# Optimization experiments

Measured on AMD Instinct MI355X. Metric: run time of the kernel, lower is better.

## Reference

```python
import jax, jax.numpy as jnp
import numpy as np

N_FFT = 1024
HOP_LENGTH = 480
NB_MAX_FRAMES = 1000
N_MELS = 64
SPEC_WIDTH = 1024
N_BINS = N_FFT // 2 + 1  # 513


def setup_inputs() -> dict:
    key = jax.random.key(0)
    B, L = 32, 480000  # 10 s @ 48 kHz -> 1001 frames, truncated to 1000
    waveform = jax.random.normal(key, (B, L), dtype=jnp.float32)

    # DFT-as-conv weights, exactly as in the torch module (hann periodic window)
    n = np.arange(N_FFT, dtype=np.float32)
    window = 0.5 - 0.5 * np.cos(2.0 * np.pi * n / N_FFT)  # torch.hann_window (periodic)
    k = np.arange(N_BINS, dtype=np.float32)[:, None]
    angle = 2.0 * np.pi * k * n[None, :] / N_FFT
    stft_weights = np.concatenate(
        [window * np.cos(angle), -window * np.sin(angle)], axis=0
    ).astype(np.float32)  # [2*N_BINS, N_FFT]

    # Stand-in for HF's slaney mel filterbank (513 -> 64): non-negative, sparse-ish scale
    mel_filters = jax.random.uniform(
        jax.random.fold_in(key, 1), (N_BINS, N_MELS), dtype=jnp.float32
    ) * 0.02

    return {
        "waveform": waveform,
        "stft_weights": jnp.asarray(stft_weights),
        "mel_filters": mel_filters,
    }


def _bilinear_align_corners(img, out_h, out_w):
    """F.interpolate(mode='bilinear', align_corners=True) on [B,C,H,W]."""
    B, C, H, W = img.shape

    def coords(out, inn):
        scale = (inn - 1) / max(out - 1, 1)
        pos = jnp.arange(out, dtype=jnp.float32) * scale
        i0 = jnp.clip(jnp.floor(pos).astype(jnp.int32), 0, inn - 1)
        return i0, pos - i0.astype(jnp.float32)

    h0, hw = coords(out_h, H)
    w0, ww = coords(out_w, W)
    h1 = jnp.minimum(h0 + 1, H - 1)
    w1 = jnp.minimum(w0 + 1, W - 1)

    rows = (img[:, :, h0, :] * (1.0 - hw)[None, None, :, None]
            + img[:, :, h1, :] * hw[None, None, :, None])  # [B,C,out_h,W]
    out = rows[..., w0] * (1.0 - ww) + rows[..., w1] * ww   # [B,C,out_h,out_w]
    return out


def reference(waveform, stft_weights, mel_filters):
    pad = N_FFT // 2
    x = jnp.pad(waveform, ((0, 0), (pad, pad)), mode="reflect")  # center=True

    # strided conv1d == frame extraction + GEMM with the DFT matrix
    T = (x.shape[1] - N_FFT) // HOP_LENGTH + 1
    idx = jnp.arange(T)[:, None] * HOP_LENGTH + jnp.arange(N_FFT)[None, :]
    frames = x[:, idx]                                   # [B, T, N_FFT]
    spec = jnp.einsum("btn,kn->bkt", frames, stft_weights)  # [B, 2*N_BINS, T]

    real = spec[:, :N_BINS, :]
    imag = spec[:, N_BINS:, :]
    power = (real * real + imag * imag)[:, :, :NB_MAX_FRAMES]  # [B, 513, 1000]

    mel = jnp.einsum("bft,fm->bmt", power, mel_filters)        # [B, 64, 1000]
    log_mel = 10.0 * jnp.log10(jnp.clip(mel, 1e-10))

    img = jnp.transpose(log_mel, (0, 2, 1))[:, None]           # [B, 1, 1000, 64]
    return _bilinear_align_corners(img, SPEC_WIDTH, N_MELS)    # [B, 1, 1024, 64]
```

## Files before the change

### kernel.cpp

```cpp
#include <hip/hip_runtime.h>
#include <hip/hip_bf16.h>
#include <math.h>

#define LWAV   480000
#define XHALF  240512
#define NBATCH 32
#define TOUT   1000
#define NMEL   64
#define PSTR   576
#define SPECW  1024

#define XPE_OFF  0u
#define XPO_OFF  15392768u
#define WEO_OFF  30785536u
#define WMT_OFF  31834112u
#define PW_OFF   31907840u
#define LM_OFF   68771840u
#define W256_OFF 76963840u

typedef __attribute__((ext_vector_type(8))) __bf16 bf16x8;
typedef __attribute__((ext_vector_type(8))) unsigned short ushort8;
typedef __attribute__((ext_vector_type(4))) float  f32x4;

__device__ __forceinline__ void gload16(const void* g, void* l) {
  __builtin_amdgcn_global_load_lds((const __attribute__((address_space(1))) void*)g,
                                   (__attribute__((address_space(3))) void*)l, 16, 0, 0);
}
#define WAIT_VM(n)  asm volatile("s_waitcnt vmcnt(" #n ")" ::: "memory")
#define WAIT_LGKM0  asm volatile("s_waitcnt lgkmcnt(0)" ::: "memory")
#define BAR() __builtin_amdgcn_s_barrier()

__device__ __forceinline__ float bf2f(unsigned short u) {
  return __uint_as_float((unsigned)u << 16);
}

#define NG1 (NBATCH * (XHALF / 8))
#define NG2 ((1024 * 512) / 8)
#define NG3 ((NMEL * PSTR) / 8)
#define NG4 (1024 / 8)

__global__ void prep_kernel(const float* __restrict__ wav,
                            const float* __restrict__ wstft,
                            const float* __restrict__ mf,
                            unsigned char* __restrict__ ws) {
  __hip_bfloat16* xpE = (__hip_bfloat16*)(ws + XPE_OFF);
  __hip_bfloat16* xpO = (__hip_bfloat16*)(ws + XPO_OFF);
  __hip_bfloat16* weo = (__hip_bfloat16*)(ws + WEO_OFF);
  __hip_bfloat16* wmt = (__hip_bfloat16*)(ws + WMT_OFF);
  __hip_bfloat16* w256 = (__hip_bfloat16*)(ws + W256_OFF);
  int idx = blockIdx.x * blockDim.x + threadIdx.x;
  if (idx < NG1) {
    int b = idx / (XHALF / 8);
    int g = idx - b * (XHALF / 8);
    const float* src = wav + (size_t)b * LWAV;
    __hip_bfloat16 e[8], o[8];
    if (g >= 32 && g <= 30030) {
      const float4* p = (const float4*)(src + 16 * g - 512);
#pragma unroll
      for (int u = 0; u < 4; ++u) {
        float4 v = p[u];
        e[2 * u]     = __float2bfloat16(v.x);
        o[2 * u]     = __float2bfloat16(v.y);
        e[2 * u + 1] = __float2bfloat16(v.z);
        o[2 * u + 1] = __float2bfloat16(v.w);
      }
    } else {
      for (int i = 0; i < 16; ++i) {
        int q = 16 * g + i;
        int s = q - 512;
        if (s < 0) s = -s;
        else if (s >= LWAV) s = 2 * (LWAV - 1) - s;
        __hip_bfloat16 v = __float2bfloat16(src[s]);
        if (i & 1) o[i >> 1] = v; else e[i >> 1] = v;
      }
    }
    *(uint4*)(xpE + (size_t)b * XHALF + 8 * g) = *(const uint4*)e;
    *(uint4*)(xpO + (size_t)b * XHALF + 8 * g) = *(const uint4*)o;
  } else if (idx < NG1 + NG2) {
    int v = idx - NG1;
    int row = v >> 6;
    int mseg = (v & 63) * 8;
    int comp = row >> 8, j = row & 255;
    __hip_bfloat16 t[8];
    if (comp < 2) {
      const float4* srow = (const float4*)(wstft + (size_t)(comp == 0 ? j : 513 + j) * 1024 + 2 * mseg);
#pragma unroll
      for (int u = 0; u < 4; ++u) {
        float4 vv = srow[u];
        t[2 * u]     = __float2bfloat16(vv.x);
        t[2 * u + 1] = __float2bfloat16(vv.z);
      }
    } else {
      const float4* w0 = (const float4*)(wstft + 2 * mseg);
#pragma unroll
      for (int u = 0; u < 4; ++u) {
        float4 wwv = w0[u];
        float wo[2] = {wwv.y, wwv.w};
#pragma unroll
        for (int h = 0; h < 2; ++h) {
          int mm = mseg + 2 * u + h;
          int q = (j * mm) & 511;
          float ang = (float)q * 0.012271846f;
          float val = (comp == 2) ? wo[h] * cosf(ang) : -wo[h] * sinf(ang);
          t[2 * u + h] = __float2bfloat16(val);
        }
      }
    }
    *(uint4*)(weo + (size_t)row * 512 + mseg) = *(const uint4*)t;
  } else if (idx < NG1 + NG2 + NG3) {
    int j = idx - NG1 - NG2;
    int n = j / (PSTR / 8);
    int k0 = (j - n * (PSTR / 8)) * 8;
    for (int k = k0; k < k0 + 8; ++k)
      wmt[n * PSTR + k] = __float2bfloat16(k < 513 ? mf[k * NMEL + n] : 0.0f);
  } else if (idx < NG1 + NG2 + NG3 + NG4) {
    int j = idx - NG1 - NG2 - NG3;
    int part = j >> 6;
    int m0 = (j & 63) * 8;
    __hip_bfloat16 t[8];
#pragma unroll
    for (int h = 0; h < 8; ++h) {
      int m = m0 + h;
      float v = part == 0 ? wstft[(size_t)256 * 1024 + 2 * m]
                          : wstft[(size_t)769 * 1024 + 2 * m + 1];
      t[h] = __float2bfloat16(v);
    }
    *(uint4*)(w256 + part * 512 + m0) = *(const uint4*)t;
  }
}

__launch_bounds__(256, 2)
__global__ void p256_kernel(unsigned char* __restrict__ ws) {
  __hip_bfloat16* pw = (__hip_bfloat16*)(ws + PW_OFF);
  const int tid  = threadIdx.x;
  const int l16  = tid & 15;
  const int fidx = blockIdx.x * 16 + (tid >> 4);
  const int b = fidx / 1000, t = fidx - b * 1000;

  const unsigned short* xe = (const unsigned short*)(ws + XPE_OFF) +
      (size_t)b * XHALF + 240 * (size_t)t + l16 * 32;
  const unsigned short* xo = (const unsigned short*)(ws + XPO_OFF) +
      (size_t)b * XHALF + 240 * (size_t)t + l16 * 32;
  const unsigned short* we = (const unsigned short*)(ws + W256_OFF) + l16 * 32;
  const unsigned short* wo = (const unsigned short*)(ws + W256_OFF) + 512 + l16 * 32;

  ushort8 ev[4], ov[4], wev[4], wov[4];
#pragma unroll
  for (int q = 0; q < 4; ++q) {
    ev[q]  = *(const ushort8*)(xe + q * 8);
    ov[q]  = *(const ushort8*)(xo + q * 8);
    wev[q] = *(const ushort8*)(we + q * 8);
    wov[q] = *(const ushort8*)(wo + q * 8);
  }
  float dc = 0.f, ds = 0.f;
#pragma unroll
  for (int q = 0; q < 4; ++q)
#pragma unroll
    for (int u = 0; u < 8; ++u) {
      dc += bf2f(ev[q][u]) * bf2f(wev[q][u]);
      ds += bf2f(ov[q][u]) * bf2f(wov[q][u]);
    }
#pragma unroll
  for (int d = 1; d < 16; d <<= 1) {
    dc += __shfl_xor(dc, d);
    ds += __shfl_xor(ds, d);
  }
  if (l16 == 0)
    pw[((size_t)b * TOUT + t) * PSTR + 256] = __float2bfloat16(dc * dc + ds * ds);
}

#define STFT_NWG 1000
__launch_bounds__(256, 2)
__global__ void stft_kernel(unsigned char* __restrict__ ws) {
  __shared__ __align__(16) unsigned char lds[65536];
  __hip_bfloat16* pw = (__hip_bfloat16*)(ws + PW_OFF);

  const int tid  = threadIdx.x;
  const int lane = tid & 63;
  const int w    = tid >> 6;
  const int wm   = w >> 1;
  const int wn   = w & 1;

  const int orig = blockIdx.x;
  const int wg = (orig & 7) * 125 + (orig >> 3);
  const int j0 = (wg & 3) * 64;
  const int m0 = (wg >> 2) * 128;

  const unsigned char* gsA[4];
  {
    int sl  = tid & 7;
    int rq  = tid >> 3;
    int slp = sl ^ (rq & 7);
#pragma unroll
    for (int i = 0; i < 4; ++i) {
      int row = i * 32 + rq;
      int m = m0 + row;
      int bb = m / 1000, tt = m - bb * 1000;
      size_t fb = ((size_t)bb * XHALF + 240 * (size_t)tt) * 2;
      gsA[i] = (slp < 4) ? (ws + XPE_OFF + fb + slp * 16)
                         : (ws + XPO_OFF + fb + (slp - 4) * 16);
    }
  }
  const unsigned char* gsB[4];
  {
    int sl2  = tid & 3;
    int rq2  = tid >> 2;
    int sl2p = sl2 ^ ((rq2 >> 1) & 3);
#pragma unroll
    for (int i = 0; i < 4; ++i) {
      int row2 = i * 64 + rq2;
      int comp = (row2 >> 4) & 3;
      int jj = j0 + (row2 >> 6) * 16 + (row2 & 15);
      gsB[i] = ws + WEO_OFF + (size_t)(comp * 256 + jj) * 1024 + sl2p * 16;
    }
  }

#define STG(c, kt) do {                                                           \
    gload16(gsA[0] + (size_t)(kt) * 64, lds + (c) * 32768 + 0 * 4096 + w * 1024); \
    gload16(gsA[1] + (size_t)(kt) * 64, lds + (c) * 32768 + 1 * 4096 + w * 1024); \
    gload16(gsA[2] + (size_t)(kt) * 64, lds + (c) * 32768 + 2 * 4096 + w * 1024); \
    gload16(gsA[3] + (size_t)(kt) * 64, lds + (c) * 32768 + 3 * 4096 + w * 1024); \
    gload16(gsB[0] + (size_t)(kt) * 64, lds + (c) * 32768 + 16384 + 0 * 4096 + w * 1024); \
    gload16(gsB[1] + (size_t)(kt) * 64, lds + (c) * 32768 + 16384 + 1 * 4096 + w * 1024); \
    gload16(gsB[2] + (size_t)(kt) * 64, lds + (c) * 32768 + 16384 + 2 * 4096 + w * 1024); \
    gload16(gsB[3] + (size_t)(kt) * 64, lds + (c) * 32768 + 16384 + 3 * 4096 + w * 1024); \
  } while (0)

  const int l15 = lane & 15, lc = lane >> 4;
  const int aoffs = (wm * 64 + l15) * 128 + ((lc ^ (l15 & 7)) << 4);
  const int boffs = 16384 + (wn * 128 + l15) * 64 + ((lc ^ ((l15 >> 1) & 3)) << 4);

  bf16x8 ae[4], ao[4], bfr[8];
  f32x4 acc[4][8];
#pragma unroll
  for (int a = 0; a < 4; ++a)
#pragma unroll
    for (int b2 = 0; b2 < 8; ++b2) acc[a][b2] = (f32x4){0.f, 0.f, 0.f, 0.f};

#define RD_ALL(C) do {                                                       \
    _Pragma("unroll")                                                        \
    for (int mf = 0; mf < 4; ++mf) {                                         \
      ae[mf] = *(const bf16x8*)(lds + (C) + aoffs + mf * 2048);              \
      ao[mf] = *(const bf16x8*)(lds + (C) + (aoffs ^ 64) + mf * 2048);       \
    }                                                                        \
    _Pragma("unroll")                                                        \
    for (int nf = 0; nf < 8; ++nf)                                           \
      bfr[nf] = *(const bf16x8*)(lds + (C) + boffs + nf * 1024);             \
  } while (0)

#define MFMA_ALL() do {                                                      \
    __builtin_amdgcn_s_setprio(1);                                           \
    _Pragma("unroll")                                                        \
    for (int mf = 0; mf < 4; ++mf)                                           \
      _Pragma("unroll")                                                      \
      for (int g = 0; g < 2; ++g) {                                          \
        acc[mf][g*4+0] = __builtin_amdgcn_mfma_f32_16x16x32_bf16(            \
            ae[mf], bfr[g*4+0], acc[mf][g*4+0], 0, 0, 0);                    \
        acc[mf][g*4+1] = __builtin_amdgcn_mfma_f32_16x16x32_bf16(            \
            ae[mf], bfr[g*4+1], acc[mf][g*4+1], 0, 0, 0);                    \
        acc[mf][g*4+2] = __builtin_amdgcn_mfma_f32_16x16x32_bf16(            \
            ao[mf], bfr[g*4+2], acc[mf][g*4+2], 0, 0, 0);                    \
        acc[mf][g*4+3] = __builtin_amdgcn_mfma_f32_16x16x32_bf16(            \
            ao[mf], bfr[g*4+3], acc[mf][g*4+3], 0, 0, 0);                    \
      }                                                                      \
    __builtin_amdgcn_s_setprio(0);                                           \
  } while (0)

  STG(0, 0);
  STG(1, 1);
  WAIT_VM(8);
  BAR();

#pragma unroll
  for (int kt = 0; kt < 16; ++kt) {
    const int c = kt & 1;
    RD_ALL(c * 32768);
    MFMA_ALL();
    if (kt == 15) break;
    WAIT_LGKM0;
    BAR();
    if (kt + 2 < 16) STG(c, kt + 2);
    if (kt < 14) { WAIT_VM(8); } else { WAIT_VM(0); }
    BAR();
  }

#pragma unroll
  for (int g = 0; g < 2; ++g) {
    int j = j0 + wn * 32 + g * 16 + l15;
    float th = (float)j * 0.0061359233f;
    float ct = cosf(th), st = sinf(th);
#pragma unroll
    for (int mf = 0; mf < 4; ++mf)
#pragma unroll
      for (int r = 0; r < 4; ++r) {
        int m = m0 + wm * 64 + mf * 16 + lc * 4 + r;
        float Ec = acc[mf][g*4+0][r], Es = acc[mf][g*4+1][r];
        float Oc = acc[mf][g*4+2][r], Os = acc[mf][g*4+3][r];
        float tOc = ct * Oc + st * Os;
        float tOs = ct * Os - st * Oc;
        float re1 = Ec + tOc, im1 = Es + tOs;
        float re2 = Ec - tOc, im2 = Es - tOs;
        pw[(size_t)m * PSTR + j]         = __float2bfloat16(re1 * re1 + im1 * im1);
        pw[(size_t)m * PSTR + (512 - j)] = __float2bfloat16(re2 * re2 + im2 * im2);
      }
  }
}

__launch_bounds__(256, 4)
__global__ void mel_kernel(unsigned char* __restrict__ ws) {
  __shared__ __align__(16) unsigned char sA[64 * 128];
  __shared__ __align__(16) unsigned char sBt[64 * 128];
  const unsigned char* pwb  = ws + PW_OFF;
  const unsigned char* wmtb = ws + WMT_OFF;
  float* lm = (float*)(ws + LM_OFF);

  const int tid = threadIdx.x;
  const int lane = tid & 63;
  const int wid  = tid >> 6;
  const int m0 = blockIdx.x * 64;

  const int strow = tid >> 3;
  const int scol  = (tid & 7) << 4;

  const unsigned char* aptr[2];
  const unsigned char* bptr[2];
  unsigned char* aldst[2];
  unsigned char* bldst[2];
#pragma unroll
  for (int jj = 0; jj < 2; ++jj) {
    int rr = jj * 32 + strow;
    aptr[jj] = pwb + (size_t)(m0 + rr) * (PSTR * 2) + (scol ^ ((rr & 7) << 4));
    bptr[jj] = wmtb + (size_t)rr * (PSTR * 2) + (scol ^ ((rr & 7) << 4));
    aldst[jj] = &sA [jj * 4096 + wid * 1024];
    bldst[jj] = &sBt[jj * 4096 + wid * 1024];
  }

  f32x4 acc[4];
#pragma unroll
  for (int fr = 0; fr < 4; ++fr) acc[fr] = (f32x4){0.f, 0.f, 0.f, 0.f};

  for (int kk = 0; kk < PSTR; kk += 64) {
    __syncthreads();
#pragma unroll
    for (int jj = 0; jj < 2; ++jj) gload16(aptr[jj] + (size_t)kk * 2, aldst[jj]);
#pragma unroll
    for (int jj = 0; jj < 2; ++jj) gload16(bptr[jj] + (size_t)kk * 2, bldst[jj]);
    __syncthreads();
#pragma unroll
    for (int ks = 0; ks < 2; ++ks) {
      const int kby = ks * 64 + ((lane >> 4) << 4);
      bf16x8 af, bfr[4];
      {
        int rr = wid * 16 + (lane & 15);
        af = *(const bf16x8*)&sA[rr * 128 + (kby ^ ((rr & 7) << 4))];
      }
#pragma unroll
      for (int fr = 0; fr < 4; ++fr) {
        int rr = fr * 16 + (lane & 15);
        bfr[fr] = *(const bf16x8*)&sBt[rr * 128 + (kby ^ ((rr & 7) << 4))];
      }
#pragma unroll
      for (int fr = 0; fr < 4; ++fr)
        acc[fr] = __builtin_amdgcn_mfma_f32_16x16x32_bf16(af, bfr[fr], acc[fr], 0, 0, 0);
    }
  }

  const int col = lane & 15;
  const int rg  = lane >> 4;
#pragma unroll
  for (int fr = 0; fr < 4; ++fr) {
    int n = fr * 16 + col;
#pragma unroll
    for (int rr = 0; rr < 4; ++rr) {
      int mrow = wid * 16 + rg * 4 + rr;
      float v = acc[fr][rr];
      lm[(size_t)(m0 + mrow) * NMEL + n] = 10.0f * log10f(fmaxf(v, 1e-10f));
    }
  }
}

__global__ void interp_kernel(const unsigned char* __restrict__ ws, float* __restrict__ out) {
  const float* lm = (const float*)(ws + LM_OFF);
  int idx = blockIdx.x * blockDim.x + threadIdx.x;
  if (idx >= NBATCH * SPECW * 16) return;
  int m4 = idx & 15;
  int h  = (idx >> 4) & (SPECW - 1);
  int b  = idx >> 14;
  const float scale = (float)(999.0 / 1023.0);
  float pos = (float)h * scale;
  int i0 = (int)floorf(pos);
  if (i0 > TOUT - 1) i0 = TOUT - 1;
  float wgt = pos - (float)i0;
  int i1 = i0 + 1;
  if (i1 > TOUT - 1) i1 = TOUT - 1;
  const float4* r0 = (const float4*)(lm + ((size_t)b * TOUT + i0) * NMEL);
  const float4* r1 = (const float4*)(lm + ((size_t)b * TOUT + i1) * NMEL);
  float4 a = r0[m4], c = r1[m4];
  float4 o;
  o.x = a.x * (1.0f - wgt) + c.x * wgt;
  o.y = a.y * (1.0f - wgt) + c.y * wgt;
  o.z = a.z * (1.0f - wgt) + c.z * wgt;
  o.w = a.w * (1.0f - wgt) + c.w * wgt;
  ((float4*)out)[idx] = o;
}

extern "C" void kernel_launch(void* const* d_in, const int* in_sizes, int n_in,
                              void* d_out, int out_size, void* d_ws, size_t ws_size,
                              hipStream_t stream) {
  (void)in_sizes; (void)n_in; (void)out_size; (void)ws_size;
  const float* wav   = (const float*)d_in[0];
  const float* wstft = (const float*)d_in[1];
  const float* mf    = (const float*)d_in[2];
  unsigned char* ws  = (unsigned char*)d_ws;
  float* out = (float*)d_out;

  const int tot = NG1 + NG2 + NG3 + NG4;
  prep_kernel<<<(tot + 255) / 256, 256, 0, stream>>>(wav, wstft, mf, ws);
  stft_kernel<<<STFT_NWG, 256, 0, stream>>>(ws);
  p256_kernel<<<2000, 256, 0, stream>>>(ws);
  mel_kernel<<<500, 256, 0, stream>>>(ws);
  interp_kernel<<<(NBATCH * SPECW * 16) / 256, 256, 0, stream>>>(ws, out);
}
```

Before: 93.77 us.

## Load STFT B operand directly from global into registers, halve LDS

Result: slower. 142.2 us (+51.6%).

```diff
diff --git a/kernel.cpp b/kernel.cpp
--- a/kernel.cpp
+++ b/kernel.cpp
@@ -172,7 +172,7 @@
 #define STFT_NWG 1000
 __launch_bounds__(256, 2)
 __global__ void stft_kernel(unsigned char* __restrict__ ws) {
-  __shared__ __align__(16) unsigned char lds[65536];
+  __shared__ __align__(16) unsigned char lds[32768];
   __hip_bfloat16* pw = (__hip_bfloat16*)(ws + PW_OFF);
 
   const int tid  = threadIdx.x;
@@ -201,87 +201,94 @@
                          : (ws + XPO_OFF + fb + (slp - 4) * 16);
     }
   }
-  const unsigned char* gsB[4];
-  {
-    int sl2  = tid & 3;
-    int rq2  = tid >> 2;
-    int sl2p = sl2 ^ ((rq2 >> 1) & 3);
-#pragma unroll
-    for (int i = 0; i < 4; ++i) {
-      int row2 = i * 64 + rq2;
-      int comp = (row2 >> 4) & 3;
-      int jj = j0 + (row2 >> 6) * 16 + (row2 & 15);
-      gsB[i] = ws + WEO_OFF + (size_t)(comp * 256 + jj) * 1024 + sl2p * 16;
-    }
-  }
-
-#define STG(c, kt) do {                                                           \
-    gload16(gsA[0] + (size_t)(kt) * 64, lds + (c) * 32768 + 0 * 4096 + w * 1024); \
-    gload16(gsA[1] + (size_t)(kt) * 64, lds + (c) * 32768 + 1 * 4096 + w * 1024); \
-    gload16(gsA[2] + (size_t)(kt) * 64, lds + (c) * 32768 + 2 * 4096 + w * 1024); \
-    gload16(gsA[3] + (size_t)(kt) * 64, lds + (c) * 32768 + 3 * 4096 + w * 1024); \
-    gload16(gsB[0] + (size_t)(kt) * 64, lds + (c) * 32768 + 16384 + 0 * 4096 + w * 1024); \
-    gload16(gsB[1] + (size_t)(kt) * 64, lds + (c) * 32768 + 16384 + 1 * 4096 + w * 1024); \
-    gload16(gsB[2] + (size_t)(kt) * 64, lds + (c) * 32768 + 16384 + 2 * 4096 + w * 1024); \
-    gload16(gsB[3] + (size_t)(kt) * 64, lds + (c) * 32768 + 16384 + 3 * 4096 + w * 1024); \
+
+#define STG_A(c, kt) do {                                                  \
+    gload16(gsA[0] + (size_t)(kt) * 64, lds + (c) * 16384 + 0 * 4096 + w * 1024); \
+    gload16(gsA[1] + (size_t)(kt) * 64, lds + (c) * 16384 + 1 * 4096 + w * 1024); \
+    gload16(gsA[2] + (size_t)(kt) * 64, lds + (c) * 16384 + 2 * 4096 + w * 1024); \
+    gload16(gsA[3] + (size_t)(kt) * 64, lds + (c) * 16384 + 3 * 4096 + w * 1024); \
   } while (0)
 
   const int l15 = lane & 15, lc = lane >> 4;
+  const unsigned char* gsBrow[8];
+#pragma unroll
+  for (int nf = 0; nf < 8; ++nf) {
+    int row2 = wn * 128 + nf * 16 + l15;
+    int comp = (row2 >> 4) & 3;
+    int jj = j0 + (row2 >> 6) * 16 + (row2 & 15);
+    gsBrow[nf] = ws + WEO_OFF + (size_t)(comp * 256 + jj) * 1024 + lc * 16;
+  }
+#define LOAD_B(dst, kt) do {                                               \
+    _Pragma("unroll")                                                      \
+    for (int nf = 0; nf < 8; ++nf)                                         \
+      dst[nf] = *(const bf16x8*)(gsBrow[nf] + (size_t)(kt) * 64);          \
+  } while (0)
+
   const int aoffs = (wm * 64 + l15) * 128 + ((lc ^ (l15 & 7)) << 4);
-  const int boffs = 16384 + (wn * 128 + l15) * 64 + ((lc ^ ((l15 >> 1) & 3)) << 4);
-
-  bf16x8 ae[4], ao[4], bfr[8];
+
+  bf16x8 ae[4], ao[4], bX[8], bY[8];
   f32x4 acc[4][8];
 #pragma unroll
   for (int a = 0; a < 4; ++a)
 #pragma unroll
     for (int b2 = 0; b2 < 8; ++b2) acc[a][b2] = (f32x4){0.f, 0.f, 0.f, 0.f};
 
-#define RD_ALL(C) do {                                                       \
-    _Pragma("unroll")                                                        \
-    for (int mf = 0; mf < 4; ++mf) {                                         \
-      ae[mf] = *(const bf16x8*)(lds + (C) + aoffs + mf * 2048);              \
-      ao[mf] = *(const bf16x8*)(lds + (C) + (aoffs ^ 64) + mf * 2048);       \
-    }                                                                        \
-    _Pragma("unroll")                                                        \
-    for (int nf = 0; nf < 8; ++nf)                                           \
-      bfr[nf] = *(const bf16x8*)(lds + (C) + boffs + nf * 1024);             \
+#define RD_A(C) do {                                                       \
+    _Pragma("unroll")                                                      \
+    for (int mf = 0; mf < 4; ++mf) {                                       \
+      ae[mf] = *(const bf16x8*)(lds + (C) + aoffs + mf * 2048);            \
+      ao[mf] = *(const bf16x8*)(lds + (C) + (aoffs ^ 64) + mf * 2048);     \
+    }                                                                      \
   } while (0)
 
-#define MFMA_ALL() do {                                                      \
-    __builtin_amdgcn_s_setprio(1);                                           \
-    _Pragma("unroll")                                                        \
-    for (int mf = 0; mf < 4; ++mf)                                           \
-      _Pragma("unroll")                                                      \
-      for (int g = 0; g < 2; ++g) {                                          \
-        acc[mf][g*4+0] = __builtin_amdgcn_mfma_f32_16x16x32_bf16(            \
-            ae[mf], bfr[g*4+0], acc[mf][g*4+0], 0, 0, 0);                    \
-        acc[mf][g*4+1] = __builtin_amdgcn_mfma_f32_16x16x32_bf16(            \
-            ae[mf], bfr[g*4+1], acc[mf][g*4+1], 0, 0, 0);                    \
-        acc[mf][g*4+2] = __builtin_amdgcn_mfma_f32_16x16x32_bf16(            \
-            ao[mf], bfr[g*4+2], acc[mf][g*4+2], 0, 0, 0);                    \
-        acc[mf][g*4+3] = __builtin_amdgcn_mfma_f32_16x16x32_bf16(            \
-            ao[mf], bfr[g*4+3], acc[mf][g*4+3], 0, 0, 0);                    \
-      }                                                                      \
-    __builtin_amdgcn_s_setprio(0);                                           \
+#define MFMA_ALL(B) do {                                                   \
+    __builtin_amdgcn_s_setprio(1);                                         \
+    _Pragma("unroll")                                                      \
+    for (int mf = 0; mf < 4; ++mf)                                         \
+      _Pragma("unroll")                                                    \
+      for (int g = 0; g < 2; ++g) {                                        \
+        acc[mf][g*4+0] = __builtin_amdgcn_mfma_f32_16x16x32_bf16(          \
+            ae[mf], B[g*4+0], acc[mf][g*4+0], 0, 0, 0);                    \
+        acc[mf][g*4+1] = __builtin_amdgcn_mfma_f32_16x16x32_bf16(          \
+            ae[mf], B[g*4+1], acc[mf][g*4+1], 0, 0, 0);                    \
+        acc[mf][g*4+2] = __builtin_amdgcn_mfma_f32_16x16x32_bf16(          \
+            ao[mf], B[g*4+2], acc[mf][g*4+2], 0, 0, 0);                    \
+        acc[mf][g*4+3] = __builtin_amdgcn_mfma_f32_16x16x32_bf16(          \
+            ao[mf], B[g*4+3], acc[mf][g*4+3], 0, 0, 0);                    \
+      }                                                                    \
+    __builtin_amdgcn_s_setprio(0);                                         \
   } while (0)
 
-  STG(0, 0);
-  STG(1, 1);
-  WAIT_VM(8);
+  STG_A(0, 0);
+  STG_A(1, 1);
+  LOAD_B(bX, 0);
+  WAIT_VM(12);
   BAR();
 
-#pragma unroll
-  for (int kt = 0; kt < 16; ++kt) {
-    const int c = kt & 1;
-    RD_ALL(c * 32768);
-    MFMA_ALL();
-    if (kt == 15) break;
+  for (int i = 0; i < 8; ++i) {
+    const bool more = (i < 7);
+    RD_A(0);
+    LOAD_B(bY, 2 * i + 1);
+    MFMA_ALL(bX);
     WAIT_LGKM0;
     BAR();
-    if (kt + 2 < 16) STG(c, kt + 2);
-    if (kt < 14) { WAIT_VM(8); } else { WAIT_VM(0); }
+    if (more) {
+      STG_A(0, (size_t)(2 * i + 2));
+      WAIT_VM(12);
+    } else {
+      WAIT_VM(8);
+    }
     BAR();
+    RD_A(16384);
+    if (more) LOAD_B(bX, 2 * i + 2);
+    MFMA_ALL(bY);
+    if (more) {
+      WAIT_LGKM0;
+      BAR();
+      STG_A(1, (size_t)(2 * i + 3));
+      WAIT_VM(12);
+      BAR();
+    }
   }
 
 #pragma unroll
```
